# Kernel optimization log

Measured on AMD Instinct MI355X. Metric: run time of the kernel, lower is better.

The kernel has to match this reference:

```python
import jax, jax.numpy as jnp
import numpy as np

B, NA, NMAX, NC = 32, 8400, 32, 80
TOPK, ALPHA, BETA, EPS, BG_IDX = 13, 1.0, 6.0, 1e-9, 80
IMG = 640.0


def _ciou(box1, box2, eps=1e-7):
    # box1: (b, nmax, 1, 4) xyxy, box2: (b, 1, na, 4) xyxy -> CIoU (b, nmax, na)
    b1_x1, b1_y1, b1_x2, b1_y2 = (box1[..., 0], box1[..., 1], box1[..., 2], box1[..., 3])
    b2_x1, b2_y1, b2_x2, b2_y2 = (box2[..., 0], box2[..., 1], box2[..., 2], box2[..., 3])
    inter = (jnp.minimum(b1_x2, b2_x2) - jnp.maximum(b1_x1, b2_x1)).clip(0) * \
            (jnp.minimum(b1_y2, b2_y2) - jnp.maximum(b1_y1, b2_y1)).clip(0)
    w1, h1 = b1_x2 - b1_x1, b1_y2 - b1_y1 + eps
    w2, h2 = b2_x2 - b2_x1, b2_y2 - b2_y1 + eps
    union = w1 * h1 + w2 * h2 - inter + eps
    iou = inter / union
    cw = jnp.maximum(b1_x2, b2_x2) - jnp.minimum(b1_x1, b2_x1)
    ch = jnp.maximum(b1_y2, b2_y2) - jnp.minimum(b1_y1, b2_y1)
    c2 = cw * cw + ch * ch + eps
    rho2 = ((b2_x1 + b2_x2 - b1_x1 - b1_x2) ** 2 + (b2_y1 + b2_y2 - b1_y1 - b1_y2) ** 2) / 4.0
    v = (4.0 / np.pi ** 2) * (jnp.arctan(w2 / h2) - jnp.arctan(w1 / h1)) ** 2
    alpha = jax.lax.stop_gradient(v / (v - iou + (1.0 + eps)))
    return iou - (rho2 / c2 + v * alpha)


def _rand_boxes(key, shape):
    # well-formed xyxy boxes inside a 640x640 image
    k1, k2 = jax.random.split(key)
    xy = jax.random.uniform(k1, shape[:-1] + (2,), jnp.float32) * (IMG - 64.0)
    wh = jax.random.uniform(k2, shape[:-1] + (2,), jnp.float32) * 56.0 + 8.0
    return jnp.concatenate([xy, xy + wh], axis=-1)


def setup_inputs() -> dict:
    key = jax.random.key(0)
    ks = jax.random.split(key, 6)
    pd_scores = jax.random.uniform(ks[0], (B, NA, NC), jnp.float32)
    pd_bboxes = _rand_boxes(ks[1], (B, NA, 4))
    anc_points = jax.random.uniform(ks[2], (NA, 2), jnp.float32) * IMG
    gt_labels = jax.random.randint(ks[3], (B, NMAX, 1), 0, NC, dtype=jnp.int32)
    gt_bboxes = _rand_boxes(ks[4], (B, NMAX, 4))
    mask_gt = jnp.ones((B, NMAX, 1), jnp.float32)
    return {"pd_scores": pd_scores, "pd_bboxes": pd_bboxes, "anc_points": anc_points,
            "gt_labels": gt_labels, "gt_bboxes": gt_bboxes, "mask_gt": mask_gt}


def reference(pd_scores, pd_bboxes, anc_points, gt_labels, gt_bboxes, mask_gt):
    b, na, nc = pd_scores.shape
    nmax = gt_bboxes.shape[1]
    # pairwise CIoU between every GT and every predicted box: (b, nmax, na)
    overlaps = _ciou(gt_bboxes[:, :, None, :], pd_bboxes[:, None, :, :])
    # gather predicted class score at each GT's label: (b, nmax, na)
    p = jnp.transpose(pd_scores, (0, 2, 1))                     # (b, nc, na)
    scores = jnp.take_along_axis(p, gt_labels.astype(jnp.int32), axis=1)
    align_metric = (scores ** ALPHA) * (overlaps ** BETA)
    # top-k anchors per GT along the anchor axis, scatter to a boolean mask
    _, topk_idx = jax.lax.top_k(align_metric, TOPK)             # (b, nmax, topk)
    bi = jnp.arange(b)[:, None, None]
    gi = jnp.arange(nmax)[None, :, None]
    mask_pos = jnp.zeros((b, nmax, na), bool).at[bi, gi, topk_idx].set(True)
    target_gt_idx = jnp.argmax(mask_pos, axis=1)                # (b, na)
    fg_mask = mask_pos.sum(axis=1) > 0                          # (b, na)
    # gather assigned GT label / box per anchor
    target_labels = jnp.take_along_axis(gt_labels[..., 0].astype(jnp.int32), target_gt_idx, axis=1)
    target_bboxes = jnp.take_along_axis(gt_bboxes, target_gt_idx[..., None], axis=1)  # (b, na, 4)
    target_scores = jax.nn.one_hot(target_labels, nc, dtype=jnp.float32) * fg_mask[..., None]
    target_labels = jnp.where(fg_mask, target_labels, BG_IDX)
    # normalize target scores by mean positive overlap per anchor, clamped to [0, 1]
    mpf = mask_pos.astype(overlaps.dtype)
    pos_overlaps = jnp.clip((overlaps * mpf).sum(axis=1) / (mpf.sum(axis=1) + EPS), 0.0, 1.0)
    target_scores = target_scores * pos_overlaps[..., None]
    return target_labels, target_bboxes, target_scores, fg_mask, target_gt_idx
```

## Files before the change

### kernel.cpp

```cpp
#include <hip/hip_runtime.h>
#include <math.h>

#define BATCH 32
#define NA 8400
#define NMAX 32
#define NC 80
#define TOPK 13
#define THREADS 256
#define NF4ROW (NA / 4)
#define NPT4 9
#define TILE 128
#define SSTRIDE 81

#define OFF_BOX 268800
#define OFF_SCR 1344000
#define OFF_FG  22848000
#define OFF_TGT 23116800
#define SCR_ELEMS (OFF_FG - OFF_SCR)
#define SCR_F4    (SCR_ELEMS / 4)
#define ZPB       (SCR_F4 / (BATCH * NMAX))

typedef float f32x4 __attribute__((ext_vector_type(4)));

__device__ __forceinline__ float ciou_f(float gx1, float gy1, float gx2, float gy2,
                                        float px1, float py1, float px2, float py2) {
    const float eps = 1e-7f;
    float iw = fmaxf(fminf(gx2, px2) - fmaxf(gx1, px1), 0.0f);
    float ih = fmaxf(fminf(gy2, py2) - fmaxf(gy1, py1), 0.0f);
    float inter = iw * ih;
    float w1 = gx2 - gx1, h1 = gy2 - gy1 + eps;
    float w2 = px2 - px1, h2 = py2 - py1 + eps;
    float uni = w1 * h1 + w2 * h2 - inter + eps;
    float iou = inter / uni;
    float cw = fmaxf(gx2, px2) - fminf(gx1, px1);
    float ch = fmaxf(gy2, py2) - fminf(gy1, py1);
    float c2 = cw * cw + ch * ch + eps;
    float dx = px1 + px2 - gx1 - gx2;
    float dy = py1 + py2 - gy1 - gy2;
    float rho2 = (dx * dx + dy * dy) / 4.0f;
    float dd = atanf(w2 / h2) - atanf(w1 / h1);
    float v = (float)(4.0 / (M_PI * M_PI)) * dd * dd;
    float alpha = v / (v - iou + (1.0f + eps));
    return iou - (rho2 / c2 + v * alpha);
}

__global__ __launch_bounds__(THREADS, 2) void metric_kernel(
    const float* __restrict__ pd_scores, const float* __restrict__ pd_bboxes,
    const int* __restrict__ gt_labels, const float* __restrict__ gt_bboxes,
    float* __restrict__ met, unsigned int* __restrict__ mask) {
    const int b = blockIdx.y;
    const int abase = blockIdx.x * TILE;
    const int tid = threadIdx.x;
    const int na_tile = min(TILE, NA - abase);
    const float eps = 1e-7f;

    if (tid < na_tile) mask[(size_t)b * NA + abase + tid] = 0u;

    __shared__ float ssc[TILE][SSTRIDE];
    __shared__ float4 spbox[TILE];
    __shared__ float sgx1[NMAX], sgy1[NMAX], sgx2[NMAX], sgy2[NMAX];
    __shared__ float sa1[NMAX], sat1[NMAX];
    __shared__ int   slbl[NMAX];

    if (tid < NMAX) {
        float4 g = ((const float4*)gt_bboxes)[b * NMAX + tid];
        float w1 = g.z - g.x, h1 = g.w - g.y + eps;
        sgx1[tid] = g.x; sgy1[tid] = g.y; sgx2[tid] = g.z; sgy2[tid] = g.w;
        sa1[tid]  = w1 * h1;
        sat1[tid] = atanf(w1 / h1);
        slbl[tid] = gt_labels[b * NMAX + tid];
    } else if (tid >= 128) {
        int al = tid - 128;
        if (al < na_tile)
            spbox[al] = ((const float4*)pd_bboxes)[(size_t)b * NA + abase + al];
    }

    const f32x4* srec4 = (const f32x4*)(pd_scores + ((size_t)b * NA + abase) * NC);
    const int nf4 = na_tile * 20;
    f32x4 r[10];
#pragma unroll
    for (int i = 0; i < 10; i++) {
        int f = tid + i * THREADS;
        if (f < nf4) r[i] = __builtin_nontemporal_load(srec4 + f);
    }
#pragma unroll
    for (int i = 0; i < 10; i++) {
        int f = tid + i * THREADS;
        if (f < nf4) {
            int a = f / 20, c = f % 20;
            float* d = &ssc[a][c * 4];
            d[0] = r[i][0]; d[1] = r[i][1]; d[2] = r[i][2]; d[3] = r[i][3];
        }
    }
    __syncthreads();

    const int al = tid & (TILE - 1);
    const int gbase = (tid >> 7) * 16;
    if (al >= na_tile) return;

    float4 p = spbox[al];
    float w2 = p.z - p.x, h2 = p.w - p.y + eps;
    float a2  = w2 * h2;
    float at2 = atanf(w2 / h2);
    const size_t abs_a = (size_t)abase + al;

#pragma unroll
    for (int k = 0; k < 16; k++) {
        int gi = gbase + k;
        float gx1 = sgx1[gi], gy1 = sgy1[gi], gx2 = sgx2[gi], gy2 = sgy2[gi];
        float iw = fmaxf(fminf(gx2, p.z) - fmaxf(gx1, p.x), 0.0f);
        float ih = fmaxf(fminf(gy2, p.w) - fmaxf(gy1, p.y), 0.0f);
        float inter = iw * ih;
        float uni = sa1[gi] + a2 - inter + eps;
        float iou = inter / uni;
        float cw = fmaxf(gx2, p.z) - fminf(gx1, p.x);
        float ch = fmaxf(gy2, p.w) - fminf(gy1, p.y);
        float c2 = cw * cw + ch * ch + eps;
        float dx = p.x + p.z - gx1 - gx2;
        float dy = p.y + p.w - gy1 - gy2;
        float rho2 = (dx * dx + dy * dy) / 4.0f;
        float dd = at2 - sat1[gi];
        float v = (float)(4.0 / (M_PI * M_PI)) * dd * dd;
        float alpha = v / (v - iou + (1.0f + eps));
        float ov = iou - (rho2 / c2 + v * alpha);
        float sc = ssc[al][slbl[gi]];
        float ov2 = ov * ov;
        met[((size_t)b * NMAX + gi) * NA + abs_a] = sc * (ov2 * ov2 * ov2);
    }
}

__global__ __launch_bounds__(THREADS) void topk_kernel(
    const float* __restrict__ met, unsigned int* __restrict__ mask,
    float* __restrict__ zbase) {
    const int tid  = threadIdx.x;
    const int lane = tid & 63;
    const int w    = tid >> 6;
    const int bid  = blockIdx.x;
    const int b  = bid >> 5;
    const int gi = bid & 31;
    const f32x4* mrow4 = (const f32x4*)(met + ((size_t)b * NMAX + gi) * NA);

    f32x4 m4[NPT4];
#pragma unroll
    for (int j = 0; j < NPT4; j++) {
        int f = j * THREADS + tid;
        if (f < NF4ROW) m4[j] = mrow4[f];
    }

    if (zbase) {
        f32x4* zp = (f32x4*)zbase + (size_t)bid * ZPB;
        const f32x4 z = { 0.f, 0.f, 0.f, 0.f };
#pragma unroll 4
        for (int i = tid; i < ZPB; i += THREADS)
            __builtin_nontemporal_store(z, zp + i);
    }

    float bv0 = -INFINITY, bv1 = -INFINITY;
    int   ba0 = 0x7FFFFFFF, ba1 = 0x7FFFFFFF;
#pragma unroll
    for (int j = 0; j < NPT4; j++) {
        int f = j * THREADS + tid;
        bool vf = (f < NF4ROW);
#pragma unroll
        for (int c = 0; c < 4; c++) {
            float v = vf ? m4[j][c] : -INFINITY;
            int   a = vf ? 4 * f + c : 0x7FFFFFFF;
            bool beats0 = (v > bv0) || (v == bv0 && a < ba0);
            bool beats1 = (v > bv1) || (v == bv1 && a < ba1);
            if (beats0) { bv1 = bv0; ba1 = ba0; bv0 = v; ba0 = a; }
            else if (beats1) { bv1 = v; ba1 = a; }
        }
    }
    bool valid1 = true;

    float rv = -INFINITY; int ra = 0x7FFFFFFF;
    for (int k = 0; k < TOPK; k++) {
        float v = bv0; int a = ba0;
#pragma unroll
        for (int s = 1; s < 64; s <<= 1) {
            float ov = __shfl_xor(v, s);
            int   oa = __shfl_xor(a, s);
            if (ov > v || (ov == v && oa < a)) { v = ov; a = oa; }
        }
        if (lane == k) { rv = v; ra = a; }
        if (ba0 == a) {
            if (valid1) { bv0 = bv1; ba0 = ba1; valid1 = false; }
            else {
                float nv = -INFINITY; int na_ = 0x7FFFFFFF;
#pragma unroll
                for (int j = 0; j < NPT4; j++) {
                    int f = j * THREADS + tid;
                    bool vf = (f < NF4ROW);
#pragma unroll
                    for (int c = 0; c < 4; c++) {
                        float mv = vf ? m4[j][c] : -INFINITY;
                        int   ma = vf ? 4 * f + c : 0x7FFFFFFF;
                        bool below = (mv < v) || (mv == v && ma > a);
                        bool beats = (mv > nv) || (mv == nv && ma < na_);
                        if (below && beats && vf) { nv = mv; na_ = ma; }
                    }
                }
                bv0 = nv; ba0 = na_;
            }
        }
    }

    __shared__ float lv[4 * TOPK];
    __shared__ int   la[4 * TOPK];
    if (lane < TOPK) { lv[w * TOPK + lane] = rv; la[w * TOPK + lane] = ra; }
    __syncthreads();

    if (w == 0) {
        float v = (lane < 4 * TOPK) ? lv[lane] : -INFINITY;
        int   a = (lane < 4 * TOPK) ? la[lane] : 0x7FFFFFFF;
        for (int k = 0; k < TOPK; k++) {
            float wv = v; int wa = a;
#pragma unroll
            for (int s = 1; s < 64; s <<= 1) {
                float ov = __shfl_xor(wv, s);
                int   oa = __shfl_xor(wa, s);
                if (ov > wv || (ov == wv && oa < wa)) { wv = ov; wa = oa; }
            }
            if (lane == 0) atomicOr(&mask[(size_t)b * NA + wa], 1u << gi);
            if (a == wa) { v = -INFINITY; a = 0x7FFFFFFF; }
        }
    }
}

__global__ __launch_bounds__(THREADS) void zero_scr_kernel(float* __restrict__ out) {
    f32x4* p = (f32x4*)(out + OFF_SCR);
    const f32x4 z = { 0.f, 0.f, 0.f, 0.f };
    const int stride = gridDim.x * THREADS;
    for (int i = blockIdx.x * THREADS + threadIdx.x; i < SCR_F4; i += stride)
        __builtin_nontemporal_store(z, p + i);
}

__global__ __launch_bounds__(THREADS) void assign_kernel(
    const float* __restrict__ pd_bboxes, const int* __restrict__ gt_labels,
    const float* __restrict__ gt_bboxes, const unsigned int* __restrict__ mask,
    float* __restrict__ out) {
    const int idx = blockIdx.x * THREADS + threadIdx.x;
    const int b = idx / NA;

    unsigned msk = mask[idx];
    int tgt = msk ? (__ffs(msk) - 1) : 0;
    float4 gb = ((const float4*)gt_bboxes)[b * NMAX + tgt];
    int lbl = gt_labels[b * NMAX + tgt];
    float4 p = ((const float4*)pd_bboxes)[idx];

    float sum = 0.0f;
    int cnt = 0;
    unsigned mm = msk;
    while (mm) {
        int i = __ffs(mm) - 1;
        mm &= mm - 1;
        float4 g = ((const float4*)gt_bboxes)[b * NMAX + i];
        sum += ciou_f(g.x, g.y, g.z, g.w, p.x, p.y, p.z, p.w);
        cnt++;
    }
    float po = fminf(fmaxf(sum / ((float)cnt + 1e-9f), 0.0f), 1.0f);

    bool fg = (msk != 0);
    __builtin_nontemporal_store(fg ? (float)lbl : 80.0f, &out[idx]);
    f32x4 gbv = { gb.x, gb.y, gb.z, gb.w };
    __builtin_nontemporal_store(gbv, (f32x4*)(out + OFF_BOX) + idx);
    __builtin_nontemporal_store(fg ? 1.0f : 0.0f, &out[OFF_FG + idx]);
    __builtin_nontemporal_store((float)tgt, &out[OFF_TGT + idx]);
    if (fg) out[OFF_SCR + (size_t)idx * NC + lbl] = po;
}

extern "C" void kernel_launch(void* const* d_in, const int* in_sizes, int n_in,
                              void* d_out, int out_size, void* d_ws, size_t ws_size,
                              hipStream_t stream) {
    const float* pd_scores = (const float*)d_in[0];
    const float* pd_bboxes = (const float*)d_in[1];
    const int*   gt_labels = (const int*)d_in[3];
    const float* gt_bboxes = (const float*)d_in[4];

    float* out = (float*)d_out;
    unsigned int* mask = (unsigned int*)d_ws;

    const size_t MASK_BYTES = (size_t)BATCH * NA * 4;
    const size_t MET_BYTES  = (size_t)BATCH * NMAX * NA * 4;
    const size_t met_off = (MASK_BYTES + 255) & ~(size_t)255;
    const bool ws_met = (ws_size >= met_off + MET_BYTES);

    float* met = ws_met ? (float*)((char*)d_ws + met_off) : out + OFF_SCR;

    dim3 g1((NA + TILE - 1) / TILE, BATCH);
    metric_kernel<<<g1, THREADS, 0, stream>>>(pd_scores, pd_bboxes,
                                              gt_labels, gt_bboxes, met, mask);
    if (ws_met) {
        topk_kernel<<<BATCH * NMAX, THREADS, 0, stream>>>(met, mask, out + OFF_SCR);
    } else {
        topk_kernel<<<BATCH * NMAX, THREADS, 0, stream>>>(met, mask, nullptr);
        zero_scr_kernel<<<2048, THREADS, 0, stream>>>(out);
    }
    assign_kernel<<<BATCH * NA / THREADS, THREADS, 0, stream>>>(
        pd_bboxes, gt_labels, gt_bboxes, mask, out);
}
```

Baseline: 87.96 us.

## Fuse metric, top-k and assign stages into one cooperative persistent kernel

Replaces the three-launch pipeline (metric, top-k, assign) with a single cooperative kernel that loops over virtual blocks and separates the phases with grid-wide syncs. The score-buffer zeroing is folded into the first phase. This removes kernel launch gaps and tail effects between stages. In exchange it adds grid.sync overhead and caps the grid to occupancy-limited size (at most 512 blocks), which may reduce parallelism in each phase. The old multi-kernel path is kept as a fallback.

```diff
diff --git a/kernel.cpp b/kernel.cpp
--- a/kernel.cpp
+++ b/kernel.cpp
@@ -1,5 +1,8 @@
 #include <hip/hip_runtime.h>
+#include <hip/hip_cooperative_groups.h>
 #include <math.h>
+
+namespace cg = cooperative_groups;
 
 #define BATCH 32
 #define NA 8400
@@ -10,6 +13,7 @@
 #define NF4ROW (NA / 4)
 #define NPT4 9
 #define TILE 128
+#define NTILES 66
 #define SSTRIDE 81
 
 #define OFF_BOX 268800
@@ -42,6 +46,227 @@
     float v = (float)(4.0 / (M_PI * M_PI)) * dd * dd;
     float alpha = v / (v - iou + (1.0f + eps));
     return iou - (rho2 / c2 + v * alpha);
+}
+
+__global__ __launch_bounds__(THREADS, 2) void fused_kernel(
+    const float* __restrict__ pd_scores, const float* __restrict__ pd_bboxes,
+    const int* __restrict__ gt_labels, const float* __restrict__ gt_bboxes,
+    float* __restrict__ met, unsigned int* __restrict__ mask,
+    float* __restrict__ out) {
+    cg::grid_group grid = cg::this_grid();
+    const int tid = threadIdx.x;
+    const float eps = 1e-7f;
+
+    __shared__ float ssc[TILE][SSTRIDE];
+    __shared__ float4 spbox[TILE];
+    __shared__ float sgx1[NMAX], sgy1[NMAX], sgx2[NMAX], sgy2[NMAX];
+    __shared__ float sa1[NMAX], sat1[NMAX];
+    __shared__ int   slbl[NMAX];
+    __shared__ float lv[4 * TOPK];
+    __shared__ int   la[4 * TOPK];
+
+    for (int vb = blockIdx.x; vb < NTILES * BATCH; vb += gridDim.x) {
+        const int b = vb / NTILES;
+        const int abase = (vb % NTILES) * TILE;
+        const int na_tile = min(TILE, NA - abase);
+
+        __syncthreads();
+
+        if (tid < na_tile) mask[(size_t)b * NA + abase + tid] = 0u;
+
+        if (tid < NMAX) {
+            float4 g = ((const float4*)gt_bboxes)[b * NMAX + tid];
+            float w1 = g.z - g.x, h1 = g.w - g.y + eps;
+            sgx1[tid] = g.x; sgy1[tid] = g.y; sgx2[tid] = g.z; sgy2[tid] = g.w;
+            sa1[tid]  = w1 * h1;
+            sat1[tid] = atanf(w1 / h1);
+            slbl[tid] = gt_labels[b * NMAX + tid];
+        } else if (tid >= 128) {
+            int al = tid - 128;
+            if (al < na_tile)
+                spbox[al] = ((const float4*)pd_bboxes)[(size_t)b * NA + abase + al];
+        }
+
+        const f32x4* srec4 = (const f32x4*)(pd_scores + ((size_t)b * NA + abase) * NC);
+        const int nf4 = na_tile * 20;
+        f32x4 r[10];
+#pragma unroll
+        for (int i = 0; i < 10; i++) {
+            int f = tid + i * THREADS;
+            if (f < nf4) r[i] = __builtin_nontemporal_load(srec4 + f);
+        }
+#pragma unroll
+        for (int i = 0; i < 10; i++) {
+            int f = tid + i * THREADS;
+            if (f < nf4) {
+                int a = f / 20, c = f % 20;
+                float* d = &ssc[a][c * 4];
+                d[0] = r[i][0]; d[1] = r[i][1]; d[2] = r[i][2]; d[3] = r[i][3];
+            }
+        }
+        __syncthreads();
+
+        const int al = tid & (TILE - 1);
+        const int gbase = (tid >> 7) * 16;
+        if (al < na_tile) {
+            float4 p = spbox[al];
+            float w2 = p.z - p.x, h2 = p.w - p.y + eps;
+            float a2  = w2 * h2;
+            float at2 = atanf(w2 / h2);
+            const size_t abs_a = (size_t)abase + al;
+#pragma unroll
+            for (int k = 0; k < 16; k++) {
+                int gi = gbase + k;
+                float gx1 = sgx1[gi], gy1 = sgy1[gi], gx2 = sgx2[gi], gy2 = sgy2[gi];
+                float iw = fmaxf(fminf(gx2, p.z) - fmaxf(gx1, p.x), 0.0f);
+                float ih = fmaxf(fminf(gy2, p.w) - fmaxf(gy1, p.y), 0.0f);
+                float inter = iw * ih;
+                float uni = sa1[gi] + a2 - inter + eps;
+                float iou = inter / uni;
+                float cw = fmaxf(gx2, p.z) - fminf(gx1, p.x);
+                float ch = fmaxf(gy2, p.w) - fminf(gy1, p.y);
+                float c2 = cw * cw + ch * ch + eps;
+                float dx = p.x + p.z - gx1 - gx2;
+                float dy = p.y + p.w - gy1 - gy2;
+                float rho2 = (dx * dx + dy * dy) / 4.0f;
+                float dd = at2 - sat1[gi];
+                float v = (float)(4.0 / (M_PI * M_PI)) * dd * dd;
+                float alpha = v / (v - iou + (1.0f + eps));
+                float ov = iou - (rho2 / c2 + v * alpha);
+                float sc = ssc[al][slbl[gi]];
+                float ov2 = ov * ov;
+                met[((size_t)b * NMAX + gi) * NA + abs_a] = sc * (ov2 * ov2 * ov2);
+            }
+        }
+    }
+
+    {
+        f32x4* zp = (f32x4*)(out + OFF_SCR);
+        const f32x4 z = { 0.f, 0.f, 0.f, 0.f };
+        const int stride = gridDim.x * THREADS;
+        for (int i = blockIdx.x * THREADS + tid; i < SCR_F4; i += stride)
+            __builtin_nontemporal_store(z, zp + i);
+    }
+
+    grid.sync();
+
+    const int lane = tid & 63;
+    const int w    = tid >> 6;
+    for (int vb = blockIdx.x; vb < BATCH * NMAX; vb += gridDim.x) {
+        const int b  = vb >> 5;
+        const int gi = vb & 31;
+        const f32x4* mrow4 = (const f32x4*)(met + ((size_t)b * NMAX + gi) * NA);
+
+        __syncthreads();
+
+        f32x4 m4[NPT4];
+#pragma unroll
+        for (int j = 0; j < NPT4; j++) {
+            int f = j * THREADS + tid;
+            if (f < NF4ROW) m4[j] = mrow4[f];
+        }
+
+        float bv0 = -INFINITY, bv1 = -INFINITY;
+        int   ba0 = 0x7FFFFFFF, ba1 = 0x7FFFFFFF;
+#pragma unroll
+        for (int j = 0; j < NPT4; j++) {
+            int f = j * THREADS + tid;
+            bool vf = (f < NF4ROW);
+#pragma unroll
+            for (int c = 0; c < 4; c++) {
+                float v = vf ? m4[j][c] : -INFINITY;
+                int   a = vf ? 4 * f + c : 0x7FFFFFFF;
+                bool beats0 = (v > bv0) || (v == bv0 && a < ba0);
+                bool beats1 = (v > bv1) || (v == bv1 && a < ba1);
+                if (beats0) { bv1 = bv0; ba1 = ba0; bv0 = v; ba0 = a; }
+                else if (beats1) { bv1 = v; ba1 = a; }
+            }
+        }
+        bool valid1 = true;
+
+        float rv = -INFINITY; int ra = 0x7FFFFFFF;
+        for (int k = 0; k < TOPK; k++) {
+            float v = bv0; int a = ba0;
+#pragma unroll
+            for (int s = 1; s < 64; s <<= 1) {
+                float ov = __shfl_xor(v, s);
+                int   oa = __shfl_xor(a, s);
+                if (ov > v || (ov == v && oa < a)) { v = ov; a = oa; }
+            }
+            if (lane == k) { rv = v; ra = a; }
+            if (ba0 == a) {
+                if (valid1) { bv0 = bv1; ba0 = ba1; valid1 = false; }
+                else {
+                    float nv = -INFINITY; int na_ = 0x7FFFFFFF;
+#pragma unroll
+                    for (int j = 0; j < NPT4; j++) {
+                        int f = j * THREADS + tid;
+                        bool vf = (f < NF4ROW);
+#pragma unroll
+                        for (int c = 0; c < 4; c++) {
+                            float mv = vf ? m4[j][c] : -INFINITY;
+                            int   ma = vf ? 4 * f + c : 0x7FFFFFFF;
+                            bool below = (mv < v) || (mv == v && ma > a);
+                            bool beats = (mv > nv) || (mv == nv && ma < na_);
+                            if (below && beats && vf) { nv = mv; na_ = ma; }
+                        }
+                    }
+                    bv0 = nv; ba0 = na_;
+                }
+            }
+        }
+
+        if (lane < TOPK) { lv[w * TOPK + lane] = rv; la[w * TOPK + lane] = ra; }
+        __syncthreads();
+
+        if (w == 0) {
+            float v = (lane < 4 * TOPK) ? lv[lane] : -INFINITY;
+            int   a = (lane < 4 * TOPK) ? la[lane] : 0x7FFFFFFF;
+            for (int k = 0; k < TOPK; k++) {
+                float wv = v; int wa = a;
+#pragma unroll
+                for (int s = 1; s < 64; s <<= 1) {
+                    float ov = __shfl_xor(wv, s);
+                    int   oa = __shfl_xor(wa, s);
+                    if (ov > wv || (ov == wv && oa < wa)) { wv = ov; wa = oa; }
+                }
+                if (lane == 0) atomicOr(&mask[(size_t)b * NA + wa], 1u << gi);
+                if (a == wa) { v = -INFINITY; a = 0x7FFFFFFF; }
+            }
+        }
+    }
+
+    grid.sync();
+
+    for (int idx = blockIdx.x * THREADS + tid; idx < BATCH * NA;
+         idx += gridDim.x * THREADS) {
+        const int b = idx / NA;
+        unsigned msk = mask[idx];
+        int tgt = msk ? (__ffs(msk) - 1) : 0;
+        float4 gb = ((const float4*)gt_bboxes)[b * NMAX + tgt];
+        int lbl = gt_labels[b * NMAX + tgt];
+        float4 p = ((const float4*)pd_bboxes)[idx];
+
+        float sum = 0.0f;
+        int cnt = 0;
+        unsigned mm = msk;
+        while (mm) {
+            int i = __ffs(mm) - 1;
+            mm &= mm - 1;
+            float4 g = ((const float4*)gt_bboxes)[b * NMAX + i];
+            sum += ciou_f(g.x, g.y, g.z, g.w, p.x, p.y, p.z, p.w);
+            cnt++;
+        }
+        float po = fminf(fmaxf(sum / ((float)cnt + 1e-9f), 0.0f), 1.0f);
+
+        bool fg = (msk != 0);
+        __builtin_nontemporal_store(fg ? (float)lbl : 80.0f, &out[idx]);
+        f32x4 gbv = { gb.x, gb.y, gb.z, gb.w };
+        __builtin_nontemporal_store(gbv, (f32x4*)(out + OFF_BOX) + idx);
+        __builtin_nontemporal_store(fg ? 1.0f : 0.0f, &out[OFF_FG + idx]);
+        __builtin_nontemporal_store((float)tgt, &out[OFF_TGT + idx]);
+        if (fg) out[OFF_SCR + (size_t)idx * NC + lbl] = po;
+    }
 }
 
 __global__ __launch_bounds__(THREADS, 2) void metric_kernel(
@@ -285,17 +510,31 @@
     const size_t met_off = (MASK_BYTES + 255) & ~(size_t)255;
     const bool ws_met = (ws_size >= met_off + MET_BYTES);
 
-    float* met = ws_met ? (float*)((char*)d_ws + met_off) : out + OFF_SCR;
-
-    dim3 g1((NA + TILE - 1) / TILE, BATCH);
-    metric_kernel<<<g1, THREADS, 0, stream>>>(pd_scores, pd_bboxes,
-                                              gt_labels, gt_bboxes, met, mask);
-    if (ws_met) {
-        topk_kernel<<<BATCH * NMAX, THREADS, 0, stream>>>(met, mask, out + OFF_SCR);
+    int occ = 0;
+    hipOccupancyMaxActiveBlocksPerMultiprocessor(&occ, (const void*)fused_kernel,
+                                                 THREADS, 0);
+    const bool coop_ok = ws_met && occ >= 1;
+
+    if (coop_ok) {
+        float* met = (float*)((char*)d_ws + met_off);
+        int grid = occ * 256;
+        if (grid > 512) grid = 512;
+        void* args[] = { (void*)&pd_scores, (void*)&pd_bboxes, (void*)&gt_labels,
+                         (void*)&gt_bboxes, (void*)&met, (void*)&mask, (void*)&out };
+        hipLaunchCooperativeKernel((const void*)fused_kernel, dim3(grid),
+                                   dim3(THREADS), args, 0, stream);
     } else {
-        topk_kernel<<<BATCH * NMAX, THREADS, 0, stream>>>(met, mask, nullptr);
-        zero_scr_kernel<<<2048, THREADS, 0, stream>>>(out);
-    }
-    assign_kernel<<<BATCH * NA / THREADS, THREADS, 0, stream>>>(
-        pd_bboxes, gt_labels, gt_bboxes, mask, out);
-}
+        float* met = ws_met ? (float*)((char*)d_ws + met_off) : out + OFF_SCR;
+        dim3 g1((NA + TILE - 1) / TILE, BATCH);
+        metric_kernel<<<g1, THREADS, 0, stream>>>(pd_scores, pd_bboxes,
+                                                  gt_labels, gt_bboxes, met, mask);
+        if (ws_met) {
+            topk_kernel<<<BATCH * NMAX, THREADS, 0, stream>>>(met, mask, out + OFF_SCR);
+        } else {
+            topk_kernel<<<BATCH * NMAX, THREADS, 0, stream>>>(met, mask, nullptr);
+            zero_scr_kernel<<<2048, THREADS, 0, stream>>>(out);
+        }
+        assign_kernel<<<BATCH * NA / THREADS, THREADS, 0, stream>>>(
+            pd_bboxes, gt_labels, gt_bboxes, mask, out);
+    }
+}
```

New measurement: 240.9 us. +173.9%, slower.
